# Kernel optimization log

Hardware: AMD Instinct MI355X
Metric: run time of the kernel (lower is better)

Reference implementation:

```python
import jax, jax.numpy as jnp
import numpy as np

B, C, D, H, W = 4, 128, 16, 16, 16
HID = 128
EPS = 1e-5


def setup_inputs() -> dict:
    key = jax.random.key(0)
    ks = jax.random.split(key, 10)
    s = 1.0 / np.sqrt(C)
    return {
        "x": jax.random.normal(ks[0], (B, C, D, H, W), dtype=jnp.float32),
        "Wq": jax.random.normal(ks[1], (HID, C), dtype=jnp.float32) * s,
        "bq": jax.random.normal(ks[2], (HID,), dtype=jnp.float32) * s,
        "Wk": jax.random.normal(ks[3], (HID, C), dtype=jnp.float32) * s,
        "bk": jax.random.normal(ks[4], (HID,), dtype=jnp.float32) * s,
        "Wv": jax.random.normal(ks[5], (HID, C), dtype=jnp.float32) * s,
        "bv": jax.random.normal(ks[6], (HID,), dtype=jnp.float32) * s,
        "bn_weight": jax.random.normal(ks[7], (HID,), dtype=jnp.float32),
        "bn_bias": jax.random.normal(ks[8], (HID,), dtype=jnp.float32),
        "gamma": jax.random.normal(ks[9], (1,), dtype=jnp.float32),
    }


def reference(x, Wq, bq, Wk, bk, Wv, bv, bn_weight, bn_bias, gamma):
    b, c, d, h, w = x.shape
    n = d * h * w
    xf = x.reshape(b, c, n)  # [B, C, N]
    # 1x1 conv3d == per-voxel linear: [B, hid, N]
    q = jnp.einsum("hc,bcn->bnh", Wq, xf) + bq  # [B, N, hid] (query permuted)
    k = jnp.einsum("hc,bcn->bhn", Wk, xf) + bk[None, :, None]  # [B, hid, N]
    v = jnp.einsum("hc,bcn->bhn", Wv, xf) + bv[None, :, None]  # [B, hid, N]
    # unscaled attention scores [B, N, N], softmax over last dim
    attn = jax.nn.softmax(jnp.einsum("bih,bhj->bij", q, k), axis=-1)
    # out[b,h,i] = sum_j v[b,h,j] * attn[b,i,j]
    out = jnp.einsum("bhj,bij->bhi", v, attn)  # [B, hid, N]
    # BatchNorm3d (training mode): per-channel stats over (B, N), biased var
    mean = jnp.mean(out, axis=(0, 2), keepdims=True)
    var = jnp.mean(jnp.square(out - mean), axis=(0, 2), keepdims=True)
    out = (out - mean) * jax.lax.rsqrt(var + EPS)
    out = out * bn_weight[None, :, None] + bn_bias[None, :, None]
    out = gamma[0] * out.reshape(b, c, d, h, w) + x
    return out
```

## Files before the change

### kernel.cpp

```cpp
#include <hip/hip_runtime.h>


#define NV 4096
#define LOG2E 1.44269504088896340736f
#define EPSV 1e-5f

typedef float f32x4 __attribute__((ext_vector_type(4)));
typedef float f32x16 __attribute__((ext_vector_type(16)));
typedef short bf16x8 __attribute__((ext_vector_type(8)));
typedef unsigned short u16x4 __attribute__((ext_vector_type(4)));
typedef unsigned short u16x8 __attribute__((ext_vector_type(8)));

static __device__ __forceinline__ unsigned short f2bf(float f) {
    union { float f; unsigned u; } v; v.f = f;
    unsigned r = v.u + 0x7FFFu + ((v.u >> 16) & 1u);
    return (unsigned short)(r >> 16);
}
static __device__ __forceinline__ float bf2f(unsigned short u) {
    union { unsigned u; float f; } v; v.u = ((unsigned)u) << 16; return v.f;
}
static __device__ __forceinline__ unsigned fbits(float f) {
    union { float f; unsigned u; } v; v.f = f; return v.u;
}

__global__ __launch_bounds__(256) void projx_kernel(
    const float* __restrict__ x,
    const float* __restrict__ Wq, const float* __restrict__ Wk,
    const float* __restrict__ Wv,
    const float* __restrict__ bq, const float* __restrict__ bk,
    const float* __restrict__ bv,
    unsigned short* __restrict__ Qb, unsigned short* __restrict__ Kb,
    unsigned short* __restrict__ Vb)
{
    __shared__ unsigned short xt[64 * 136];
    __shared__ unsigned short Wl[128 * 136];
    const int bid = blockIdx.x;
    const int m = bid >> 8, b = (bid >> 6) & 3, n0 = (bid & 63) << 6;
    const int t = threadIdx.x, w = t >> 6, lane = t & 63;
    const int quad = lane >> 4, l16 = lane & 15;

    const float* Wm = (m == 0) ? Wq : ((m == 1) ? Wk : Wv);
    const float* bias = (m == 0) ? bq : ((m == 1) ? bk : bv);

    #pragma unroll
    for (int it = 0; it < 8; ++it) {
        const int e = (it << 8) + t;
        const int c = e >> 4, i4 = (e & 15) << 2;
        const float4 xv = *(const float4*)(x + (((b << 7) + c) << 12) + n0 + i4);
        xt[(i4 + 0) * 136 + c] = f2bf(xv.x);
        xt[(i4 + 1) * 136 + c] = f2bf(xv.y);
        xt[(i4 + 2) * 136 + c] = f2bf(xv.z);
        xt[(i4 + 3) * 136 + c] = f2bf(xv.w);
    }
    #pragma unroll
    for (int it = 0; it < 16; ++it) {
        const int idx = it * 1024 + (t << 2);
        const float4 wv4 = *(const float4*)(Wm + idx);
        const int h = idx >> 7, c = idx & 127;
        u16x4 pk;
        pk[0] = f2bf(wv4.x); pk[1] = f2bf(wv4.y);
        pk[2] = f2bf(wv4.z); pk[3] = f2bf(wv4.w);
        *(u16x4*)(Wl + h * 136 + c) = pk;
    }
    __syncthreads();

    bf16x8 af[4];
    {
        const int il = (w << 4) + l16;
        #pragma unroll
        for (int ck = 0; ck < 4; ++ck)
            af[ck] = *(const bf16x8*)(xt + il * 136 + (ck << 5) + (quad << 3));
    }
    if (m == 2) __syncthreads();

    #pragma unroll
    for (int s = 0; s < 8; ++s) {
        const int h = (s << 4) + l16;
        f32x4 acc = {0.f, 0.f, 0.f, 0.f};
        #pragma unroll
        for (int ck = 0; ck < 4; ++ck) {
            const bf16x8 wf = *(const bf16x8*)(Wl + h * 136 + (ck << 5) + (quad << 3));
            acc = __builtin_amdgcn_mfma_f32_16x16x32_bf16(af[ck], wf, acc, 0, 0, 0);
        }
        const float bval = bias[h];
        if (m == 2) {
            #pragma unroll
            for (int r = 0; r < 4; ++r)
                xt[h * 66 + (w << 4) + (quad << 2) + r] = f2bf(acc[r] + bval);
        } else {
            #pragma unroll
            for (int r = 0; r < 4; ++r) {
                float val = acc[r] + bval;
                if (m == 0) val *= LOG2E;
                xt[((w << 4) + (quad << 2) + r) * 136 + h] = f2bf(val);
            }
        }
    }
    __syncthreads();
    if (m == 2) {
        #pragma unroll
        for (int it = 0; it < 32; ++it) {
            const int e = it * 256 + t;
            const int h = e >> 6, il = e & 63;
            Vb[(((b << 7) + h) << 12) + n0 + il] = xt[h * 66 + il];
        }
    } else {
        unsigned short* dst = (m == 0) ? Qb : Kb;
        #pragma unroll
        for (int it = 0; it < 4; ++it) {
            const int e = (it << 8) + t;
            const int row = e >> 4, c8 = (e & 15) << 3;
            *(bf16x8*)(dst + (((b << 12) + n0 + row) << 7) + c8) =
                *(const bf16x8*)(xt + row * 136 + c8);
        }
    }
}

template<int NSL>
__global__ __launch_bounds__(256, 2) void flash_kernel(
    const unsigned short* __restrict__ Qb,
    const unsigned short* __restrict__ Kb,
    const unsigned short* __restrict__ Vb,
    unsigned short* __restrict__ Opart, float* __restrict__ lpart,
    unsigned short* __restrict__ Obuf)
{
    __shared__ unsigned short Kt[64 * 128];
    __shared__ unsigned short Vt[128 * 64];
    constexpr int NB = NSL * 128;
    const int bid = ((blockIdx.x & 7) * (NB >> 3)) + (blockIdx.x >> 3);
    const int sl = bid >> 7, b = (bid >> 5) & 3, ic = bid & 31;
    const int t = threadIdx.x, w = t >> 6, lane = t & 63;
    const int l32 = lane & 31, hi = lane >> 5;
    const int iw = (ic << 7) + (w << 5);

    const int T = (NV / NSL) >> 6;
    const int jbase = sl * T << 6;

    const int ktg = t & 15, ktj = t >> 4;
    const int vtg = t & 7,  vth = t >> 3;
    const int kswz = (ktg ^ ktj) << 3;
    const int vswz = (vtg ^ (vth & 7)) << 3;

    bf16x8 qf[8];
    {
        const unsigned short* qp = Qb + (((b << 12) + iw + l32) << 7) + (hi << 3);
        #pragma unroll
        for (int kc = 0; kc < 8; ++kc) qf[kc] = *(const bf16x8*)(qp + (kc << 4));
    }
    f32x16 Oacc[4];
    #pragma unroll
    for (int ht = 0; ht < 4; ++ht)
        #pragma unroll
        for (int r = 0; r < 16; ++r) Oacc[ht][r] = 0.f;
    float lsum = 0.f;

    const unsigned short* Kbb = Kb + ((long)b << 19);
    const unsigned short* Vbb = Vb + ((long)b << 19);

    bf16x8 sk[4], sv[4];
    #pragma unroll
    for (int r = 0; r < 4; ++r)
        sk[r] = *(const bf16x8*)(Kbb + ((jbase + (r << 4) + ktj) << 7) + (ktg << 3));
    #pragma unroll
    for (int r = 0; r < 4; ++r)
        sv[r] = *(const bf16x8*)(Vbb + (((r << 5) + vth) << 12) + jbase + (vtg << 3));

    for (int t8 = 0; t8 < T; ++t8) {
        const int j0 = jbase + (t8 << 6);

        __syncthreads();
        #pragma unroll
        for (int r = 0; r < 4; ++r)
            *(bf16x8*)(Kt + (((r << 4) + ktj) << 7) + kswz) = sk[r];
        #pragma unroll
        for (int r = 0; r < 4; ++r)
            *(bf16x8*)(Vt + (((r << 5) + vth) << 6) + vswz) = sv[r];
        __syncthreads();

        if (t8 + 1 < T) {
            const int j1 = j0 + 64;
            #pragma unroll
            for (int r = 0; r < 4; ++r)
                sk[r] = *(const bf16x8*)(Kbb + ((j1 + (r << 4) + ktj) << 7) + (ktg << 3));
            #pragma unroll
            for (int r = 0; r < 4; ++r)
                sv[r] = *(const bf16x8*)(Vbb + (((r << 5) + vth) << 12) + j1 + (vtg << 3));
        }

        #pragma unroll
        for (int jt = 0; jt < 2; ++jt) {
            const unsigned short* kr = Kt + (((jt << 5) + l32) << 7);
            f32x16 a;
            #pragma unroll
            for (int r = 0; r < 16; ++r) a[r] = 0.f;
            __builtin_amdgcn_s_setprio(1);
            #pragma unroll
            for (int kc = 0; kc < 8; ++kc) {
                const bf16x8 kf = *(const bf16x8*)(kr + ((((kc << 1) + hi) ^ (l32 & 15)) << 3));
                a = __builtin_amdgcn_mfma_f32_32x32x16_bf16(kf, qf[kc], a, 0, 0, 0);
            }
            __builtin_amdgcn_s_setprio(0);
            float e[16];
            #pragma unroll
            for (int r = 0; r < 16; ++r) e[r] = __builtin_amdgcn_exp2f(a[r]);
            lsum += ((e[0] + e[1]) + (e[2] + e[3])) + ((e[4] + e[5]) + (e[6] + e[7]))
                  + ((e[8] + e[9]) + (e[10] + e[11])) + ((e[12] + e[13]) + (e[14] + e[15]));
            unsigned wd[8];
            #pragma unroll
            for (int g = 0; g < 8; ++g)
                wd[g] = __builtin_amdgcn_perm(fbits(e[2 * g + 1]), fbits(e[2 * g]),
                                              0x07060302u);
            unsigned a0 = wd[0], a2 = wd[2];
            asm("v_permlane32_swap_b32 %0, %1" : "+v"(a0), "+v"(a2));
            unsigned a1 = wd[1], a3 = wd[3];
            asm("v_permlane32_swap_b32 %0, %1" : "+v"(a1), "+v"(a3));
            unsigned b0 = wd[4], b2 = wd[6];
            asm("v_permlane32_swap_b32 %0, %1" : "+v"(b0), "+v"(b2));
            unsigned b1 = wd[5], b3 = wd[7];
            asm("v_permlane32_swap_b32 %0, %1" : "+v"(b1), "+v"(b3));
            union PW { unsigned w[4]; bf16x8 v; };
            PW p0, p1;
            p0.w[0] = a0; p0.w[1] = a1; p0.w[2] = a2; p0.w[3] = a3;
            p1.w[0] = b0; p1.w[1] = b1; p1.w[2] = b2; p1.w[3] = b3;
            const bf16x8 pa0 = p0.v, pa1 = p1.v;
            __builtin_amdgcn_s_setprio(1);
            #pragma unroll
            for (int ht = 0; ht < 4; ++ht) {
                const unsigned short* vr = Vt + (((ht << 5) + l32) << 6);
                const bf16x8 v0 = *(const bf16x8*)(vr + ((((jt << 2) + hi) ^ (l32 & 7)) << 3));
                const bf16x8 v1 = *(const bf16x8*)(vr + ((((jt << 2) + 2 + hi) ^ (l32 & 7)) << 3));
                Oacc[ht] = __builtin_amdgcn_mfma_f32_32x32x16_bf16(v0, pa0, Oacc[ht], 0, 0, 0);
                Oacc[ht] = __builtin_amdgcn_mfma_f32_32x32x16_bf16(v1, pa1, Oacc[ht], 0, 0, 0);
            }
            __builtin_amdgcn_s_setprio(0);
        }
    }

    float l = lsum;
    l += __shfl_xor(l, 32);

    if (NSL == 1) {
        const float rl = 1.f / l;
        #pragma unroll
        for (int ht = 0; ht < 4; ++ht)
            #pragma unroll
            for (int r = 0; r < 16; ++r) {
                const int h = (ht << 5) + (hi << 2) + (r & 3) + ((r >> 2) << 3);
                Obuf[(((b << 7) + h) << 12) + iw + l32] = f2bf(Oacc[ht][r] * rl);
            }
    } else {
        const int slb = (sl << 2) + b;
        if (!hi) lpart[(slb << 12) + iw + l32] = l;
        unsigned short* Ob = Opart + ((long)slb << 19);
        #pragma unroll
        for (int ht = 0; ht < 4; ++ht)
            #pragma unroll
            for (int r = 0; r < 16; ++r) {
                const int h = (ht << 5) + (hi << 2) + (r & 3) + ((r >> 2) << 3);
                Ob[(h << 12) + iw + l32] = f2bf(Oacc[ht][r]);
            }
    }
}

template<int NSL>
__global__ __launch_bounds__(1024) void mf_kernel(
    const unsigned short* __restrict__ Opart, const float* __restrict__ lpart,
    const float* __restrict__ x, const float* __restrict__ bnw,
    const float* __restrict__ bnb, const float* __restrict__ gammap,
    float* __restrict__ out)
{
    const int h = blockIdx.x;
    const int t = threadIdx.x;
    const int b = t >> 8;
    const int i0 = (t & 255) << 4;

    float A[16], L[16];
    #pragma unroll
    for (int k = 0; k < 16; ++k) { A[k] = 0.f; L[k] = 0.f; }
    #pragma unroll
    for (int sl = 0; sl < NSL; ++sl) {
        const int slb = (sl << 2) + b;
        const u16x8 u0 = *(const u16x8*)(Opart + ((long)slb << 19) + ((long)h << 12) + i0);
        const u16x8 u1 = *(const u16x8*)(Opart + ((long)slb << 19) + ((long)h << 12) + i0 + 8);
        const float* lp = lpart + (slb << 12) + i0;
        #pragma unroll
        for (int k = 0; k < 8; ++k) { A[k] += bf2f(u0[k]); A[8 + k] += bf2f(u1[k]); }
        #pragma unroll
        for (int k = 0; k < 4; ++k) {
            const float4 lv = *(const float4*)(lp + (k << 2));
            L[(k << 2) + 0] += lv.x; L[(k << 2) + 1] += lv.y;
            L[(k << 2) + 2] += lv.z; L[(k << 2) + 3] += lv.w;
        }
    }
    float o[16], s = 0.f, ss = 0.f;
    #pragma unroll
    for (int k = 0; k < 16; ++k) {
        o[k] = A[k] / L[k];
        s += o[k]; ss += o[k] * o[k];
    }
    #pragma unroll
    for (int off = 32; off; off >>= 1) {
        s  += __shfl_down(s, off);
        ss += __shfl_down(ss, off);
    }
    __shared__ float rs[16], rss[16], fin[2];
    const int wid = t >> 6;
    if ((t & 63) == 0) { rs[wid] = s; rss[wid] = ss; }
    __syncthreads();
    if (t == 0) {
        float s2 = 0.f, ss2 = 0.f;
        #pragma unroll
        for (int k = 0; k < 16; ++k) { s2 += rs[k]; ss2 += rss[k]; }
        fin[0] = s2; fin[1] = ss2;
    }
    __syncthreads();
    const float inv = 1.f / 16384.f;
    const float mean = fin[0] * inv;
    const float var  = fin[1] * inv - mean * mean;
    const float g = gammap[0];
    const float scale = bnw[h] * rsqrtf(var + EPSV);
    const float a  = g * scale;
    const float bb = g * (bnb[h] - mean * scale);

    const float* xp = x + (((b << 7) + h) << 12) + i0;
    float* op = out + (((b << 7) + h) << 12) + i0;
    #pragma unroll
    for (int k = 0; k < 4; ++k) {
        const float4 xv = *(const float4*)(xp + (k << 2));
        float4 r;
        r.x = o[(k << 2) + 0] * a + bb + xv.x;
        r.y = o[(k << 2) + 1] * a + bb + xv.y;
        r.z = o[(k << 2) + 2] * a + bb + xv.z;
        r.w = o[(k << 2) + 3] * a + bb + xv.w;
        *(float4*)(op + (k << 2)) = r;
    }
}

__global__ __launch_bounds__(1024) void mf1_kernel(
    const unsigned short* __restrict__ Obuf,
    const float* __restrict__ x, const float* __restrict__ bnw,
    const float* __restrict__ bnb, const float* __restrict__ gammap,
    float* __restrict__ out)
{
    const int h = blockIdx.x;
    const int t = threadIdx.x;
    const int b = t >> 8;
    const int i0 = (t & 255) << 4;
    const u16x8 u0 = *(const u16x8*)(Obuf + (((b << 7) + h) << 12) + i0);
    const u16x8 u1 = *(const u16x8*)(Obuf + (((b << 7) + h) << 12) + i0 + 8);
    float o[16], s = 0.f, ss = 0.f;
    #pragma unroll
    for (int k = 0; k < 8; ++k) { o[k] = bf2f(u0[k]); o[8 + k] = bf2f(u1[k]); }
    #pragma unroll
    for (int k = 0; k < 16; ++k) { s += o[k]; ss += o[k] * o[k]; }
    #pragma unroll
    for (int off = 32; off; off >>= 1) {
        s  += __shfl_down(s, off);
        ss += __shfl_down(ss, off);
    }
    __shared__ float rs[16], rss[16], fin[2];
    const int wid = t >> 6;
    if ((t & 63) == 0) { rs[wid] = s; rss[wid] = ss; }
    __syncthreads();
    if (t == 0) {
        float s2 = 0.f, ss2 = 0.f;
        #pragma unroll
        for (int k = 0; k < 16; ++k) { s2 += rs[k]; ss2 += rss[k]; }
        fin[0] = s2; fin[1] = ss2;
    }
    __syncthreads();
    const float inv = 1.f / 16384.f;
    const float mean = fin[0] * inv;
    const float var  = fin[1] * inv - mean * mean;
    const float g = gammap[0];
    const float scale = bnw[h] * rsqrtf(var + EPSV);
    const float a  = g * scale;
    const float bb = g * (bnb[h] - mean * scale);
    const float* xp = x + (((b << 7) + h) << 12) + i0;
    float* op = out + (((b << 7) + h) << 12) + i0;
    #pragma unroll
    for (int k = 0; k < 4; ++k) {
        const float4 xv = *(const float4*)(xp + (k << 2));
        float4 r;
        r.x = o[(k << 2) + 0] * a + bb + xv.x;
        r.y = o[(k << 2) + 1] * a + bb + xv.y;
        r.z = o[(k << 2) + 2] * a + bb + xv.z;
        r.w = o[(k << 2) + 3] * a + bb + xv.w;
        *(float4*)(op + (k << 2)) = r;
    }
}

extern "C" void kernel_launch(void* const* d_in, const int* in_sizes, int n_in,
                              void* d_out, int out_size, void* d_ws, size_t ws_size,
                              hipStream_t stream) {
    const float* x   = (const float*)d_in[0];
    const float* Wq  = (const float*)d_in[1];
    const float* bq  = (const float*)d_in[2];
    const float* Wk  = (const float*)d_in[3];
    const float* bk  = (const float*)d_in[4];
    const float* Wv  = (const float*)d_in[5];
    const float* bv  = (const float*)d_in[6];
    const float* bnw = (const float*)d_in[7];
    const float* bnb = (const float*)d_in[8];
    const float* gam = (const float*)d_in[9];
    float* out = (float*)d_out;

    char* ws = (char*)d_ws;
    unsigned short* Obuf = (unsigned short*)(ws);
    unsigned short* Qb   = (unsigned short*)(ws + (4u  << 20));
    unsigned short* Kb   = (unsigned short*)(ws + (8u  << 20));
    unsigned short* Vb   = (unsigned short*)(ws + (12u << 20));
    float*          lpart = (float*)(ws + (16u << 20) + (128u << 10));
    unsigned short* Opart = (unsigned short*)(ws + (17u << 20));

    int nsl = 1;
    if      (ws_size >= (17ull << 20) + (16ull << 20)) nsl = 4;
    else if (ws_size >= (17ull << 20) + (8ull  << 20)) nsl = 2;

    projx_kernel<<<768, 256, 0, stream>>>(x, Wq, Wk, Wv, bq, bk, bv, Qb, Kb, Vb);
    if (nsl == 4) {
        flash_kernel<4><<<512, 256, 0, stream>>>(Qb, Kb, Vb, Opart, lpart, Obuf);
        mf_kernel<4><<<128, 1024, 0, stream>>>(Opart, lpart, x, bnw, bnb, gam, out);
    } else if (nsl == 2) {
        flash_kernel<2><<<256, 256, 0, stream>>>(Qb, Kb, Vb, Opart, lpart, Obuf);
        mf_kernel<2><<<128, 1024, 0, stream>>>(Opart, lpart, x, bnw, bnb, gam, out);
    } else {
        flash_kernel<1><<<128, 256, 0, stream>>>(Qb, Kb, Vb, Opart, lpart, Obuf);
        mf1_kernel<<<128, 1024, 0, stream>>>(Obuf, x, bnw, bnb, gam, out);
    }
}
```

Measured before the change: 140.0 us.

## Process two 32-row query tiles per wave to reuse K/V fragments

Each wave now handles 64 query rows (two 32-row MFMA tiles) instead of 32, so every K and V fragment read from LDS feeds two MFMAs. This halves the number of blocks and drops the launch-bounds occupancy hint from 2 to 1, trading occupancy and register pressure for fewer LDS reads and global K/V loads per unit of work. The softmax/pack logic is factored into a helper that is called once per tile. With fewer blocks (256 for the 4-slice path), some CUs on a large GPU may sit idle.

```diff
diff --git a/kernel.cpp b/kernel.cpp
--- a/kernel.cpp
+++ b/kernel.cpp
@@ -21,6 +21,34 @@
 }
 static __device__ __forceinline__ unsigned fbits(float f) {
     union { float f; unsigned u; } v; v.f = f; return v.u;
+}
+
+static __device__ __forceinline__ void softmax_pack(
+    const f32x16& a, float& lsum, bf16x8& paLo, bf16x8& paHi)
+{
+    float e[16];
+    #pragma unroll
+    for (int r = 0; r < 16; ++r) e[r] = __builtin_amdgcn_exp2f(a[r]);
+    lsum += ((e[0] + e[1]) + (e[2] + e[3])) + ((e[4] + e[5]) + (e[6] + e[7]))
+          + ((e[8] + e[9]) + (e[10] + e[11])) + ((e[12] + e[13]) + (e[14] + e[15]));
+    unsigned wd[8];
+    #pragma unroll
+    for (int g = 0; g < 8; ++g)
+        wd[g] = __builtin_amdgcn_perm(fbits(e[2 * g + 1]), fbits(e[2 * g]),
+                                      0x07060302u);
+    unsigned a0 = wd[0], a2 = wd[2];
+    asm("v_permlane32_swap_b32 %0, %1" : "+v"(a0), "+v"(a2));
+    unsigned a1 = wd[1], a3 = wd[3];
+    asm("v_permlane32_swap_b32 %0, %1" : "+v"(a1), "+v"(a3));
+    unsigned b0 = wd[4], b2 = wd[6];
+    asm("v_permlane32_swap_b32 %0, %1" : "+v"(b0), "+v"(b2));
+    unsigned b1 = wd[5], b3 = wd[7];
+    asm("v_permlane32_swap_b32 %0, %1" : "+v"(b1), "+v"(b3));
+    union PW { unsigned w[4]; bf16x8 v; };
+    PW p0, p1;
+    p0.w[0] = a0; p0.w[1] = a1; p0.w[2] = a2; p0.w[3] = a3;
+    p1.w[0] = b0; p1.w[1] = b1; p1.w[2] = b2; p1.w[3] = b3;
+    paLo = p0.v; paHi = p1.v;
 }
 
 __global__ __launch_bounds__(256) void projx_kernel(
@@ -117,7 +145,7 @@
 }
 
 template<int NSL>
-__global__ __launch_bounds__(256, 2) void flash_kernel(
+__global__ __launch_bounds__(256, 1) void flash_kernel(
     const unsigned short* __restrict__ Qb,
     const unsigned short* __restrict__ Kb,
     const unsigned short* __restrict__ Vb,
@@ -126,33 +154,37 @@
 {
     __shared__ unsigned short Kt[64 * 128];
     __shared__ unsigned short Vt[128 * 64];
-    constexpr int NB = NSL * 128;
+    constexpr int NB = NSL * 64;
     const int bid = ((blockIdx.x & 7) * (NB >> 3)) + (blockIdx.x >> 3);
-    const int sl = bid >> 7, b = (bid >> 5) & 3, ic = bid & 31;
+    const int sl = bid >> 6, b = (bid >> 4) & 3, ic = bid & 15;
     const int t = threadIdx.x, w = t >> 6, lane = t & 63;
     const int l32 = lane & 31, hi = lane >> 5;
-    const int iw = (ic << 7) + (w << 5);
+    const int iw = (ic << 8) + (w << 6);
 
     const int T = (NV / NSL) >> 6;
-    const int jbase = sl * T << 6;
+    const int jbase = (sl * T) << 6;
 
     const int ktg = t & 15, ktj = t >> 4;
     const int vtg = t & 7,  vth = t >> 3;
     const int kswz = (ktg ^ ktj) << 3;
     const int vswz = (vtg ^ (vth & 7)) << 3;
 
-    bf16x8 qf[8];
+    bf16x8 qf0[8], qf1[8];
     {
-        const unsigned short* qp = Qb + (((b << 12) + iw + l32) << 7) + (hi << 3);
-        #pragma unroll
-        for (int kc = 0; kc < 8; ++kc) qf[kc] = *(const bf16x8*)(qp + (kc << 4));
-    }
-    f32x16 Oacc[4];
+        const unsigned short* qp0 = Qb + (((b << 12) + iw + l32) << 7) + (hi << 3);
+        const unsigned short* qp1 = qp0 + (32 << 7);
+        #pragma unroll
+        for (int kc = 0; kc < 8; ++kc) {
+            qf0[kc] = *(const bf16x8*)(qp0 + (kc << 4));
+            qf1[kc] = *(const bf16x8*)(qp1 + (kc << 4));
+        }
+    }
+    f32x16 Oacc0[4], Oacc1[4];
     #pragma unroll
     for (int ht = 0; ht < 4; ++ht)
         #pragma unroll
-        for (int r = 0; r < 16; ++r) Oacc[ht][r] = 0.f;
-    float lsum = 0.f;
+        for (int r = 0; r < 16; ++r) { Oacc0[ht][r] = 0.f; Oacc1[ht][r] = 0.f; }
+    float lsum0 = 0.f, lsum1 = 0.f;
 
     const unsigned short* Kbb = Kb + ((long)b << 19);
     const unsigned short* Vbb = Vb + ((long)b << 19);
@@ -190,74 +222,62 @@
         #pragma unroll
         for (int jt = 0; jt < 2; ++jt) {
             const unsigned short* kr = Kt + (((jt << 5) + l32) << 7);
-            f32x16 a;
-            #pragma unroll
-            for (int r = 0; r < 16; ++r) a[r] = 0.f;
+            f32x16 a0, a1;
+            #pragma unroll
+            for (int r = 0; r < 16; ++r) { a0[r] = 0.f; a1[r] = 0.f; }
             __builtin_amdgcn_s_setprio(1);
             #pragma unroll
             for (int kc = 0; kc < 8; ++kc) {
                 const bf16x8 kf = *(const bf16x8*)(kr + ((((kc << 1) + hi) ^ (l32 & 15)) << 3));
-                a = __builtin_amdgcn_mfma_f32_32x32x16_bf16(kf, qf[kc], a, 0, 0, 0);
+                a0 = __builtin_amdgcn_mfma_f32_32x32x16_bf16(kf, qf0[kc], a0, 0, 0, 0);
+                a1 = __builtin_amdgcn_mfma_f32_32x32x16_bf16(kf, qf1[kc], a1, 0, 0, 0);
             }
             __builtin_amdgcn_s_setprio(0);
-            float e[16];
-            #pragma unroll
-            for (int r = 0; r < 16; ++r) e[r] = __builtin_amdgcn_exp2f(a[r]);
-            lsum += ((e[0] + e[1]) + (e[2] + e[3])) + ((e[4] + e[5]) + (e[6] + e[7]))
-                  + ((e[8] + e[9]) + (e[10] + e[11])) + ((e[12] + e[13]) + (e[14] + e[15]));
-            unsigned wd[8];
-            #pragma unroll
-            for (int g = 0; g < 8; ++g)
-                wd[g] = __builtin_amdgcn_perm(fbits(e[2 * g + 1]), fbits(e[2 * g]),
-                                              0x07060302u);
-            unsigned a0 = wd[0], a2 = wd[2];
-            asm("v_permlane32_swap_b32 %0, %1" : "+v"(a0), "+v"(a2));
-            unsigned a1 = wd[1], a3 = wd[3];
-            asm("v_permlane32_swap_b32 %0, %1" : "+v"(a1), "+v"(a3));
-            unsigned b0 = wd[4], b2 = wd[6];
-            asm("v_permlane32_swap_b32 %0, %1" : "+v"(b0), "+v"(b2));
-            unsigned b1 = wd[5], b3 = wd[7];
-            asm("v_permlane32_swap_b32 %0, %1" : "+v"(b1), "+v"(b3));
-            union PW { unsigned w[4]; bf16x8 v; };
-            PW p0, p1;
-            p0.w[0] = a0; p0.w[1] = a1; p0.w[2] = a2; p0.w[3] = a3;
-            p1.w[0] = b0; p1.w[1] = b1; p1.w[2] = b2; p1.w[3] = b3;
-            const bf16x8 pa0 = p0.v, pa1 = p1.v;
+            bf16x8 pa00, pa01, pa10, pa11;
+            softmax_pack(a0, lsum0, pa00, pa01);
+            softmax_pack(a1, lsum1, pa10, pa11);
             __builtin_amdgcn_s_setprio(1);
             #pragma unroll
             for (int ht = 0; ht < 4; ++ht) {
                 const unsigned short* vr = Vt + (((ht << 5) + l32) << 6);
                 const bf16x8 v0 = *(const bf16x8*)(vr + ((((jt << 2) + hi) ^ (l32 & 7)) << 3));
                 const bf16x8 v1 = *(const bf16x8*)(vr + ((((jt << 2) + 2 + hi) ^ (l32 & 7)) << 3));
-                Oacc[ht] = __builtin_amdgcn_mfma_f32_32x32x16_bf16(v0, pa0, Oacc[ht], 0, 0, 0);
-                Oacc[ht] = __builtin_amdgcn_mfma_f32_32x32x16_bf16(v1, pa1, Oacc[ht], 0, 0, 0);
+                Oacc0[ht] = __builtin_amdgcn_mfma_f32_32x32x16_bf16(v0, pa00, Oacc0[ht], 0, 0, 0);
+                Oacc0[ht] = __builtin_amdgcn_mfma_f32_32x32x16_bf16(v1, pa01, Oacc0[ht], 0, 0, 0);
+                Oacc1[ht] = __builtin_amdgcn_mfma_f32_32x32x16_bf16(v0, pa10, Oacc1[ht], 0, 0, 0);
+                Oacc1[ht] = __builtin_amdgcn_mfma_f32_32x32x16_bf16(v1, pa11, Oacc1[ht], 0, 0, 0);
             }
             __builtin_amdgcn_s_setprio(0);
         }
     }
 
-    float l = lsum;
-    l += __shfl_xor(l, 32);
+    float l0 = lsum0; l0 += __shfl_xor(l0, 32);
+    float l1 = lsum1; l1 += __shfl_xor(l1, 32);
 
     if (NSL == 1) {
-        const float rl = 1.f / l;
+        const float rl0 = 1.f / l0, rl1 = 1.f / l1;
         #pragma unroll
         for (int ht = 0; ht < 4; ++ht)
             #pragma unroll
             for (int r = 0; r < 16; ++r) {
                 const int h = (ht << 5) + (hi << 2) + (r & 3) + ((r >> 2) << 3);
-                Obuf[(((b << 7) + h) << 12) + iw + l32] = f2bf(Oacc[ht][r] * rl);
+                Obuf[(((b << 7) + h) << 12) + iw + l32]      = f2bf(Oacc0[ht][r] * rl0);
+                Obuf[(((b << 7) + h) << 12) + iw + 32 + l32] = f2bf(Oacc1[ht][r] * rl1);
             }
     } else {
         const int slb = (sl << 2) + b;
-        if (!hi) lpart[(slb << 12) + iw + l32] = l;
+        if (!hi) {
+            lpart[(slb << 12) + iw + l32]      = l0;
+            lpart[(slb << 12) + iw + 32 + l32] = l1;
+        }
         unsigned short* Ob = Opart + ((long)slb << 19);
         #pragma unroll
         for (int ht = 0; ht < 4; ++ht)
             #pragma unroll
             for (int r = 0; r < 16; ++r) {
                 const int h = (ht << 5) + (hi << 2) + (r & 3) + ((r >> 2) << 3);
-                Ob[(h << 12) + iw + l32] = f2bf(Oacc[ht][r]);
+                Ob[(h << 12) + iw + l32]      = f2bf(Oacc0[ht][r]);
+                Ob[(h << 12) + iw + 32 + l32] = f2bf(Oacc1[ht][r]);
             }
     }
 }
@@ -419,13 +439,13 @@
 
     projx_kernel<<<768, 256, 0, stream>>>(x, Wq, Wk, Wv, bq, bk, bv, Qb, Kb, Vb);
     if (nsl == 4) {
-        flash_kernel<4><<<512, 256, 0, stream>>>(Qb, Kb, Vb, Opart, lpart, Obuf);
+        flash_kernel<4><<<256, 256, 0, stream>>>(Qb, Kb, Vb, Opart, lpart, Obuf);
         mf_kernel<4><<<128, 1024, 0, stream>>>(Opart, lpart, x, bnw, bnb, gam, out);
     } else if (nsl == 2) {
-        flash_kernel<2><<<256, 256, 0, stream>>>(Qb, Kb, Vb, Opart, lpart, Obuf);
+        flash_kernel<2><<<128, 256, 0, stream>>>(Qb, Kb, Vb, Opart, lpart, Obuf);
         mf_kernel<2><<<128, 1024, 0, stream>>>(Opart, lpart, x, bnw, bnb, gam, out);
     } else {
-        flash_kernel<1><<<128, 256, 0, stream>>>(Qb, Kb, Vb, Opart, lpart, Obuf);
+        flash_kernel<1><<<64, 256, 0, stream>>>(Qb, Kb, Vb, Opart, lpart, Obuf);
         mf1_kernel<<<128, 1024, 0, stream>>>(Obuf, x, bnw, bnb, gam, out);
     }
 }
```

Result: slower. 145.7 us (+4.0%).
